# Performance work log

Hardware: AMD Instinct MI355X
Metric: run time of the kernel (lower is better)

Reference implementation:

```python
import jax, jax.numpy as jnp
import numpy as np

B, N, D, H, K, R = 128, 2048, 256, 16, 32, 16
LEAKY_SLOPE = 0.01


def setup_inputs() -> dict:
    key = jax.random.key(0)
    ks = jax.random.split(key, 8)
    s = 0.05
    inp = jax.random.normal(ks[0], (B * N, D), dtype=jnp.float32)
    batch_ids = jnp.repeat(jnp.arange(B, dtype=jnp.int32), N)  # equal-size graphs
    Wk = jax.random.normal(ks[1], (K, D), dtype=jnp.float32) * s
    Wq0 = jax.random.normal(ks[2], (H * K, D), dtype=jnp.float32) * s
    Wq1 = jax.random.normal(ks[3], (H * K, D), dtype=jnp.float32) * s
    We = jax.random.normal(ks[4], (R, D), dtype=jnp.float32) * s
    Wout = jax.random.normal(ks[5], (D, H * R), dtype=jnp.float32) * s
    bout = jax.random.normal(ks[6], (D,), dtype=jnp.float32) * s
    return {"inp": inp, "batch_ids": batch_ids, "Wk": Wk, "Wq0": Wq0,
            "Wq1": Wq1, "We": We, "Wout": Wout, "bout": bout}


def reference(inp, batch_ids, Wk, Wq0, Wq1, We, Wout, bout):
    b = int(jnp.max(batch_ids)) + 1  # number of graphs (static at trace time)
    d = inp.shape[-1]
    # global max pool per graph (torch_geometric global_max_pool)
    pooled = jax.ops.segment_max(inp, batch_ids, num_segments=b)  # [B, D]
    x = inp.reshape(b, -1, d)                                     # [B, N, D]
    keys = jnp.einsum('bnd,kd->bnk', x, Wk)                       # [B, N, K]

    def head_embed(Wq):
        q = (pooled @ Wq.T).reshape(b, H, K)                      # [B, H, K]
        logits = jnp.einsum('bhk,bnk->bhn', q, keys)              # [B, H, N]
        att = jax.nn.softmax(logits, axis=-1)
        feat = jnp.einsum('bhn,bnd->bhd', att, x)                 # [B, H, D]
        return jnp.einsum('bhd,rd->bhr', feat, We)                # [B, H, R]

    dx = (head_embed(Wq0) - head_embed(Wq1)).reshape(b, -1)       # [B, H*R]
    out = dx @ Wout.T + bout
    return jnp.where(out >= 0, out, LEAKY_SLOPE * out)            # LeakyReLU
```

## Files before the change

### kernel.cpp

```cpp
#include <hip/hip_runtime.h>
#include <math.h>

#define B_ 128
#define N_ 2048
#define D_ 256
#define NHEADS 32

#define POOLED_OFF 0
#define PHI_OFF    32768
#define PLO_OFF    557056
#define ML_OFF     1081344
#define FEATP_OFF  1114112
#define XHI_OFF    5308416
#define XLO_OFF    38862848

#define XHI_S 0
#define XLO_S 32768
#define ATT_S 0
#define XT_S  33280
#define STAT_S 53760

typedef __attribute__((ext_vector_type(8))) short short8;
typedef __attribute__((ext_vector_type(4))) float f32x4;

__device__ __forceinline__ void atomic_max_f32(float* addr, float v) {
    if (v >= 0.0f) atomicMax((int*)addr, __float_as_int(v + 0.0f));
    else           atomicMin((unsigned int*)addr, __float_as_uint(v));
}
__device__ __forceinline__ unsigned short f2bf(float f) {
    unsigned u = __float_as_uint(f);
    u += 0x7fff + ((u >> 16) & 1);
    return (unsigned short)(u >> 16);
}
__device__ __forceinline__ float bf2f(unsigned short h) {
    return __uint_as_float(((unsigned)h) << 16);
}
__device__ __forceinline__ unsigned pack2bf(float a, float b) {
    return (unsigned)f2bf(a) | ((unsigned)f2bf(b) << 16);
}

__global__ __launch_bounds__(256) void k_init(float* __restrict__ pooled) {
    pooled[blockIdx.x * 256 + threadIdx.x] = -INFINITY;
}

__global__ __launch_bounds__(256) void k_pool(const float* __restrict__ inp,
                                              float* __restrict__ pooled,
                                              unsigned short* __restrict__ xhi,
                                              unsigned short* __restrict__ xlo) {
    int b = blockIdx.x >> 4;
    int ch = blockIdx.x & 15;
    int t = threadIdx.x;
    int sub = t >> 6;
    int dq = (t & 63) * 4;
    const float* p = inp + ((size_t)(b * N_ + ch * 128 + sub)) * D_ + dq;
    size_t nodebase = (size_t)b * N_ + ch * 128 + sub;
    float4 m = {-INFINITY, -INFINITY, -INFINITY, -INFINITY};
#pragma unroll 4
    for (int i = 0; i < 32; ++i) {
        float4 v = *(const float4*)(p + (size_t)i * 4 * D_);
        m.x = fmaxf(m.x, v.x); m.y = fmaxf(m.y, v.y);
        m.z = fmaxf(m.z, v.z); m.w = fmaxf(m.w, v.w);
        size_t node = nodebase + (size_t)i * 4;
        ushort4 h4, l4;
        h4.x = f2bf(v.x); l4.x = f2bf(v.x - bf2f(h4.x));
        h4.y = f2bf(v.y); l4.y = f2bf(v.y - bf2f(h4.y));
        h4.z = f2bf(v.z); l4.z = f2bf(v.z - bf2f(h4.z));
        h4.w = f2bf(v.w); l4.w = f2bf(v.w - bf2f(h4.w));
        *(ushort4*)(xhi + node * D_ + dq) = h4;
        *(ushort4*)(xlo + node * D_ + dq) = l4;
    }
    __shared__ float sm[4 * 256];
    sm[sub * 256 + dq + 0] = m.x;
    sm[sub * 256 + dq + 1] = m.y;
    sm[sub * 256 + dq + 2] = m.z;
    sm[sub * 256 + dq + 3] = m.w;
    __syncthreads();
    float v = fmaxf(fmaxf(sm[t], sm[256 + t]), fmaxf(sm[512 + t], sm[768 + t]));
    atomic_max_f32(pooled + b * D_ + t, v);
}

__global__ __launch_bounds__(256) void k_qp(const float* __restrict__ pooled,
                                            const float* __restrict__ Wq0,
                                            const float* __restrict__ Wq1,
                                            const float* __restrict__ Wk,
                                            unsigned short* __restrict__ Phi,
                                            unsigned short* __restrict__ Plo) {
    __shared__ float pl[D_];
    __shared__ float ql[1024];
    int b = blockIdx.x, t = threadIdx.x;
    pl[t] = pooled[b * D_ + t];
    __syncthreads();
    for (int rep = 0; rep < 4; ++rep) {
        int idx = rep * 256 + t;
        const float* Wq = (idx < 512) ? Wq0 : Wq1;
        int row = idx & 511;
        const float4* wr = (const float4*)(Wq + (size_t)row * D_);
        float acc = 0.0f;
        for (int dqi = 0; dqi < 64; ++dqi) {
            float4 w = wr[dqi];
            const float* pp = &pl[dqi * 4];
            acc += w.x * pp[0] + w.y * pp[1] + w.z * pp[2] + w.w * pp[3];
        }
        ql[idx] = acc;
    }
    __syncthreads();
    float wk[32];
#pragma unroll
    for (int k = 0; k < 32; ++k) wk[k] = Wk[k * D_ + t];
    for (int j = 0; j < NHEADS; ++j) {
        const float* q = &ql[(j >> 4) * 512 + (j & 15) * 32];
        float acc = 0.0f;
#pragma unroll
        for (int k = 0; k < 32; ++k) acc = fmaf(q[k], wk[k], acc);
        unsigned short hi = f2bf(acc);
        unsigned short lo = f2bf(acc - bf2f(hi));
        Phi[((size_t)b * NHEADS + j) * D_ + t] = hi;
        Plo[((size_t)b * NHEADS + j) * D_ + t] = lo;
    }
}

__global__ __launch_bounds__(256) void k_attn(const unsigned short* __restrict__ xhi,
                                              const unsigned short* __restrict__ xlo,
                                              const unsigned short* __restrict__ Phi,
                                              const unsigned short* __restrict__ Plo,
                                              float* __restrict__ ml,
                                              float* __restrict__ featp) {
    __shared__ uint4 smem4[4096];
    unsigned char* smem = (unsigned char*)smem4;
    float* smax = (float*)(smem + STAT_S);
    float* ssum = (float*)(smem + STAT_S + 512);

    int b = blockIdx.x >> 2, ns = blockIdx.x & 3;
    int t = threadIdx.x;
    int w = t >> 6;
    int lane = t & 63;
    int lq = lane >> 4;
    int lm = lane & 15;
    size_t gnode0 = (size_t)b * N_ + ns * 512;

    f32x4 acc_s[8][2];
#pragma unroll
    for (int mt = 0; mt < 8; ++mt)
#pragma unroll
        for (int ht = 0; ht < 2; ++ht) acc_s[mt][ht] = (f32x4){0.f, 0.f, 0.f, 0.f};

    int srow = t >> 2, sseg = t & 3;
    for (int dc = 0; dc < 8; ++dc) {
        int d0 = dc * 32;
        short8 bh[2], bl[2];
#pragma unroll
        for (int ht = 0; ht < 2; ++ht) {
            size_t poff = ((size_t)b * NHEADS + ht * 16 + lm) * D_ + d0 + lq * 8;
            bh[ht] = *(const short8*)(Phi + poff);
            bl[ht] = *(const short8*)(Plo + poff);
        }
        const unsigned short* gxh = xhi + (gnode0 + srow) * D_ + d0 + sseg * 8;
        const unsigned short* gxl = xlo + (gnode0 + srow) * D_ + d0 + sseg * 8;
        __syncthreads();
#pragma unroll
        for (int i = 0; i < 8; ++i) {
            *(uint4*)(smem + XHI_S + (size_t)(srow + i * 64) * 64 + sseg * 16) =
                *(const uint4*)(gxh + (size_t)i * 64 * D_);
            *(uint4*)(smem + XLO_S + (size_t)(srow + i * 64) * 64 + sseg * 16) =
                *(const uint4*)(gxl + (size_t)i * 64 * D_);
        }
        __syncthreads();
#pragma unroll
        for (int mt = 0; mt < 8; ++mt) {
            size_t roff = (size_t)(w * 128 + mt * 16 + lm) * 64 + lq * 16;
            short8 ah = *(const short8*)(smem + XHI_S + roff);
            short8 al = *(const short8*)(smem + XLO_S + roff);
#pragma unroll
            for (int ht = 0; ht < 2; ++ht) {
                acc_s[mt][ht] = __builtin_amdgcn_mfma_f32_16x16x32_bf16(ah, bh[ht], acc_s[mt][ht], 0, 0, 0);
                acc_s[mt][ht] = __builtin_amdgcn_mfma_f32_16x16x32_bf16(ah, bl[ht], acc_s[mt][ht], 0, 0, 0);
                acc_s[mt][ht] = __builtin_amdgcn_mfma_f32_16x16x32_bf16(al, bh[ht], acc_s[mt][ht], 0, 0, 0);
            }
        }
    }
    __syncthreads();

    float bm[2];
#pragma unroll
    for (int ht = 0; ht < 2; ++ht) {
        float m = -INFINITY;
#pragma unroll
        for (int mt = 0; mt < 8; ++mt) {
            m = fmaxf(m, fmaxf(fmaxf(acc_s[mt][ht][0], acc_s[mt][ht][1]),
                               fmaxf(acc_s[mt][ht][2], acc_s[mt][ht][3])));
        }
        m = fmaxf(m, __shfl_xor(m, 16));
        m = fmaxf(m, __shfl_xor(m, 32));
        if (lane < 16) smax[w * 32 + ht * 16 + lane] = m;
    }
    __syncthreads();
#pragma unroll
    for (int ht = 0; ht < 2; ++ht) {
        bm[ht] = fmaxf(fmaxf(smax[0 * 32 + ht * 16 + lm], smax[1 * 32 + ht * 16 + lm]),
                       fmaxf(smax[2 * 32 + ht * 16 + lm], smax[3 * 32 + ht * 16 + lm]));
    }
#pragma unroll
    for (int ht = 0; ht < 2; ++ht) {
        float s = 0.0f;
#pragma unroll
        for (int mt = 0; mt < 8; ++mt) {
            float e0 = __expf(acc_s[mt][ht][0] - bm[ht]);
            float e1 = __expf(acc_s[mt][ht][1] - bm[ht]);
            float e2 = __expf(acc_s[mt][ht][2] - bm[ht]);
            float e3 = __expf(acc_s[mt][ht][3] - bm[ht]);
            s += (e0 + e1) + (e2 + e3);
            uint2 pk;
            pk.x = pack2bf(e0, e1);
            pk.y = pack2bf(e2, e3);
            *(uint2*)(smem + ATT_S + (size_t)(ht * 16 + lm) * 1040 +
                      (size_t)(w * 128 + mt * 16 + lq * 4) * 2) = pk;
        }
        s += __shfl_xor(s, 16);
        s += __shfl_xor(s, 32);
        if (lane < 16) ssum[w * 32 + ht * 16 + lane] = s;
    }
    __syncthreads();
    if (t < 32) {
        float mB = fmaxf(fmaxf(smax[t], smax[32 + t]), fmaxf(smax[64 + t], smax[96 + t]));
        float l = ssum[t] + ssum[32 + t] + ssum[64 + t] + ssum[96 + t];
        float* mlp = ml + (((size_t)b * NHEADS + t) * 4 + ns) * 2;
        mlp[0] = mB;
        mlp[1] = l;
    }
    __syncthreads();

    f32x4 acc_o[2][4];
#pragma unroll
    for (int mt = 0; mt < 2; ++mt)
#pragma unroll
        for (int dt = 0; dt < 4; ++dt) acc_o[mt][dt] = (f32x4){0.f, 0.f, 0.f, 0.f};

    int db = t & 31, nb = t >> 5;
    for (int c = 0; c < 16; ++c) {
        const unsigned short* gx = xhi + (gnode0 + c * 32 + nb * 4) * D_ + db * 8;
        uint4 R0 = *(const uint4*)(gx);
        uint4 R1 = *(const uint4*)(gx + D_);
        uint4 R2 = *(const uint4*)(gx + 2 * D_);
        uint4 R3 = *(const uint4*)(gx + 3 * D_);
        const unsigned* r0 = (const unsigned*)&R0;
        const unsigned* r1 = (const unsigned*)&R1;
        const unsigned* r2 = (const unsigned*)&R2;
        const unsigned* r3 = (const unsigned*)&R3;
        uint2 T[8];
#pragma unroll
        for (int c2 = 0; c2 < 4; ++c2) {
            T[2 * c2 + 0].x = __builtin_amdgcn_perm(r1[c2], r0[c2], 0x05040100u);
            T[2 * c2 + 0].y = __builtin_amdgcn_perm(r3[c2], r2[c2], 0x05040100u);
            T[2 * c2 + 1].x = __builtin_amdgcn_perm(r1[c2], r0[c2], 0x07060302u);
            T[2 * c2 + 1].y = __builtin_amdgcn_perm(r3[c2], r2[c2], 0x07060302u);
        }
        __syncthreads();
#pragma unroll
        for (int j = 0; j < 8; ++j) {
            int jj = (j + db) & 7;
            *(uint2*)(smem + XT_S + (size_t)(db * 8 + jj) * 80 + nb * 8) = T[jj];
        }
        __syncthreads();
        short8 a0 = *(const short8*)(smem + ATT_S + (size_t)lm * 1040 + (size_t)(c * 32 + lq * 8) * 2);
        short8 a1 = *(const short8*)(smem + ATT_S + (size_t)(16 + lm) * 1040 + (size_t)(c * 32 + lq * 8) * 2);
#pragma unroll
        for (int dt = 0; dt < 4; ++dt) {
            short8 bf = *(const short8*)(smem + XT_S + (size_t)(w * 64 + dt * 16 + lm) * 80 + lq * 16);
            acc_o[0][dt] = __builtin_amdgcn_mfma_f32_16x16x32_bf16(a0, bf, acc_o[0][dt], 0, 0, 0);
            acc_o[1][dt] = __builtin_amdgcn_mfma_f32_16x16x32_bf16(a1, bf, acc_o[1][dt], 0, 0, 0);
        }
    }
    float* fb = featp + ((size_t)(ns * B_ + b)) * D_ * NHEADS;
#pragma unroll
    for (int mt = 0; mt < 2; ++mt)
#pragma unroll
        for (int dt = 0; dt < 4; ++dt) {
            int d = w * 64 + dt * 16 + lm;
            int h0 = mt * 16 + lq * 4;
            *(f32x4*)(fb + (size_t)d * NHEADS + h0) = acc_o[mt][dt];
        }
}

__global__ __launch_bounds__(256) void k_out(const float* __restrict__ featp,
                                             const float* __restrict__ ml,
                                             const float* __restrict__ We,
                                             const float* __restrict__ Wout,
                                             const float* __restrict__ bout,
                                             float* __restrict__ out) {
    __shared__ float f[NHEADS * 257];
    __shared__ float bhrs[512];
    __shared__ float dxs[256];
    __shared__ float wns[4 * 32];
    __shared__ float linv2[32];
    int b = blockIdx.x, t = threadIdx.x;
    if (t < 32) {
        const float* mlb = ml + ((size_t)b * NHEADS + t) * 8;
        float M = fmaxf(fmaxf(mlb[0], mlb[2]), fmaxf(mlb[4], mlb[6]));
        float e0 = __expf(mlb[0] - M), e1 = __expf(mlb[2] - M);
        float e2 = __expf(mlb[4] - M), e3 = __expf(mlb[6] - M);
        float L = e0 * mlb[1] + e1 * mlb[3] + e2 * mlb[5] + e3 * mlb[7];
        wns[0 * 32 + t] = e0; wns[1 * 32 + t] = e1;
        wns[2 * 32 + t] = e2; wns[3 * 32 + t] = e3;
        linv2[t] = 1.0f / L;
    }
    __syncthreads();
    float fj[32];
#pragma unroll
    for (int j = 0; j < 32; ++j) fj[j] = 0.0f;
#pragma unroll
    for (int ns = 0; ns < 4; ++ns) {
        const float* fp = featp + ((size_t)(ns * B_ + b) * D_ + t) * NHEADS;
#pragma unroll
        for (int j4 = 0; j4 < 8; ++j4) {
            float4 v = *(const float4*)(fp + j4 * 4);
            fj[j4 * 4 + 0] += wns[ns * 32 + j4 * 4 + 0] * v.x;
            fj[j4 * 4 + 1] += wns[ns * 32 + j4 * 4 + 1] * v.y;
            fj[j4 * 4 + 2] += wns[ns * 32 + j4 * 4 + 2] * v.z;
            fj[j4 * 4 + 3] += wns[ns * 32 + j4 * 4 + 3] * v.w;
        }
    }
#pragma unroll
    for (int j = 0; j < 32; ++j) f[j * 257 + t] = fj[j] * linv2[j];
    __syncthreads();
    for (int rep = 0; rep < 2; ++rep) {
        int idx = rep * 256 + t;
        int j = idx >> 4, r = idx & 15;
        const float* wrow = We + (size_t)r * D_;
        const float* ff = &f[j * 257];
        float acc = 0.0f;
        for (int d = 0; d < D_; ++d) acc = fmaf(ff[d], wrow[d], acc);
        bhrs[idx] = acc;
    }
    __syncthreads();
    {
        int h = t >> 4, r = t & 15;
        dxs[t] = bhrs[h * 16 + r] - bhrs[(16 + h) * 16 + r];
    }
    __syncthreads();
    float acc = bout[t];
    const float* wrow = Wout + (size_t)t * 256;
    for (int c = 0; c < 256; ++c) acc = fmaf(dxs[c], wrow[c], acc);
    out[(size_t)b * D_ + t] = acc >= 0.0f ? acc : 0.01f * acc;
}

extern "C" void kernel_launch(void* const* d_in, const int* in_sizes, int n_in,
                              void* d_out, int out_size, void* d_ws, size_t ws_size,
                              hipStream_t stream) {
    const float* inp  = (const float*)d_in[0];
    const float* Wk   = (const float*)d_in[2];
    const float* Wq0  = (const float*)d_in[3];
    const float* Wq1  = (const float*)d_in[4];
    const float* We   = (const float*)d_in[5];
    const float* Wout = (const float*)d_in[6];
    const float* bout = (const float*)d_in[7];
    float* out = (float*)d_out;
    float* ws  = (float*)d_ws;
    float* pooled = ws + POOLED_OFF;
    unsigned short* Phi = (unsigned short*)(ws + PHI_OFF);
    unsigned short* Plo = (unsigned short*)(ws + PLO_OFF);
    float* ml     = ws + ML_OFF;
    float* featp  = ws + FEATP_OFF;
    unsigned short* xhi = (unsigned short*)(ws + XHI_OFF);
    unsigned short* xlo = (unsigned short*)(ws + XLO_OFF);

    k_init<<<dim3(128), dim3(256), 0, stream>>>(pooled);
    k_pool<<<dim3(2048), dim3(256), 0, stream>>>(inp, pooled, xhi, xlo);
    k_qp<<<dim3(128), dim3(256), 0, stream>>>(pooled, Wq0, Wq1, Wk, Phi, Plo);
    k_attn<<<dim3(512), dim3(256), 0, stream>>>(xhi, xlo, Phi, Plo, ml, featp);
    k_out<<<dim3(128), dim3(256), 0, stream>>>(featp, ml, We, Wout, bout, out);
}
```

Baseline: 607.2 us.

## Fuse bf16 split into attention kernel and drop global xhi/xlo buffers

The attention kernel now reads the fp32 input directly and splits it into bf16 hi/lo parts inside a swizzled LDS tile. This removes the large global write and re-read of the xhi/xlo intermediates. Work is split into 16 chunks of 128 nodes per graph with 512-thread blocks and about 141 KB of dynamic LDS, which likely allows only one block per CU. Pooling writes per-chunk partial maxima that k_qp reduces, replacing the atomics and the init kernel. The cost is a 4x larger featp partial buffer and scalar strided LDS reads for the transposed operand.

```diff
diff --git a/kernel.cpp b/kernel.cpp
--- a/kernel.cpp
+++ b/kernel.cpp
@@ -5,28 +5,25 @@
 #define N_ 2048
 #define D_ 256
 #define NHEADS 32
-
-#define POOLED_OFF 0
-#define PHI_OFF    32768
-#define PLO_OFF    557056
-#define ML_OFF     1081344
-#define FEATP_OFF  1114112
-#define XHI_OFF    5308416
-#define XLO_OFF    38862848
-
-#define XHI_S 0
-#define XLO_S 32768
-#define ATT_S 0
-#define XT_S  33280
-#define STAT_S 53760
+#define CHUNK 128
+#define NCH 16
+
+#define POOLEDP_OFF 0
+#define PHI_OFF     524288
+#define PLO_OFF     1048576
+#define ML_OFF      1572864
+#define FEATP_OFF   1703936
+
+#define XHI_S  0
+#define XLO_S  65536
+#define ATT_S  131072
+#define SMAX_S 139776
+#define SSUM_S 140800
+#define LDS_BYTES 141824
 
 typedef __attribute__((ext_vector_type(8))) short short8;
 typedef __attribute__((ext_vector_type(4))) float f32x4;
 
-__device__ __forceinline__ void atomic_max_f32(float* addr, float v) {
-    if (v >= 0.0f) atomicMax((int*)addr, __float_as_int(v + 0.0f));
-    else           atomicMin((unsigned int*)addr, __float_as_uint(v));
-}
 __device__ __forceinline__ unsigned short f2bf(float f) {
     unsigned u = __float_as_uint(f);
     u += 0x7fff + ((u >> 16) & 1);
@@ -38,36 +35,24 @@
 __device__ __forceinline__ unsigned pack2bf(float a, float b) {
     return (unsigned)f2bf(a) | ((unsigned)f2bf(b) << 16);
 }
-
-__global__ __launch_bounds__(256) void k_init(float* __restrict__ pooled) {
-    pooled[blockIdx.x * 256 + threadIdx.x] = -INFINITY;
+__device__ __forceinline__ unsigned xsw(int row) {
+    return (unsigned)((row ^ (row >> 3)) & 7) << 4;
 }
 
 __global__ __launch_bounds__(256) void k_pool(const float* __restrict__ inp,
-                                              float* __restrict__ pooled,
-                                              unsigned short* __restrict__ xhi,
-                                              unsigned short* __restrict__ xlo) {
+                                              float* __restrict__ pooledp) {
     int b = blockIdx.x >> 4;
     int ch = blockIdx.x & 15;
     int t = threadIdx.x;
     int sub = t >> 6;
     int dq = (t & 63) * 4;
     const float* p = inp + ((size_t)(b * N_ + ch * 128 + sub)) * D_ + dq;
-    size_t nodebase = (size_t)b * N_ + ch * 128 + sub;
     float4 m = {-INFINITY, -INFINITY, -INFINITY, -INFINITY};
 #pragma unroll 4
     for (int i = 0; i < 32; ++i) {
         float4 v = *(const float4*)(p + (size_t)i * 4 * D_);
         m.x = fmaxf(m.x, v.x); m.y = fmaxf(m.y, v.y);
         m.z = fmaxf(m.z, v.z); m.w = fmaxf(m.w, v.w);
-        size_t node = nodebase + (size_t)i * 4;
-        ushort4 h4, l4;
-        h4.x = f2bf(v.x); l4.x = f2bf(v.x - bf2f(h4.x));
-        h4.y = f2bf(v.y); l4.y = f2bf(v.y - bf2f(h4.y));
-        h4.z = f2bf(v.z); l4.z = f2bf(v.z - bf2f(h4.z));
-        h4.w = f2bf(v.w); l4.w = f2bf(v.w - bf2f(h4.w));
-        *(ushort4*)(xhi + node * D_ + dq) = h4;
-        *(ushort4*)(xlo + node * D_ + dq) = l4;
     }
     __shared__ float sm[4 * 256];
     sm[sub * 256 + dq + 0] = m.x;
@@ -76,10 +61,10 @@
     sm[sub * 256 + dq + 3] = m.w;
     __syncthreads();
     float v = fmaxf(fmaxf(sm[t], sm[256 + t]), fmaxf(sm[512 + t], sm[768 + t]));
-    atomic_max_f32(pooled + b * D_ + t, v);
-}
-
-__global__ __launch_bounds__(256) void k_qp(const float* __restrict__ pooled,
+    pooledp[((size_t)ch * B_ + b) * 256 + t] = v;
+}
+
+__global__ __launch_bounds__(256) void k_qp(const float* __restrict__ pooledp,
                                             const float* __restrict__ Wq0,
                                             const float* __restrict__ Wq1,
                                             const float* __restrict__ Wk,
@@ -88,7 +73,11 @@
     __shared__ float pl[D_];
     __shared__ float ql[1024];
     int b = blockIdx.x, t = threadIdx.x;
-    pl[t] = pooled[b * D_ + t];
+    float pv = -INFINITY;
+#pragma unroll
+    for (int i = 0; i < 16; ++i)
+        pv = fmaxf(pv, pooledp[((size_t)i * B_ + b) * 256 + t]);
+    pl[t] = pv;
     __syncthreads();
     for (int rep = 0; rep < 4; ++rep) {
         int idx = rep * 256 + t;
@@ -119,76 +108,69 @@
     }
 }
 
-__global__ __launch_bounds__(256) void k_attn(const unsigned short* __restrict__ xhi,
-                                              const unsigned short* __restrict__ xlo,
-                                              const unsigned short* __restrict__ Phi,
-                                              const unsigned short* __restrict__ Plo,
-                                              float* __restrict__ ml,
-                                              float* __restrict__ featp) {
-    __shared__ uint4 smem4[4096];
-    unsigned char* smem = (unsigned char*)smem4;
-    float* smax = (float*)(smem + STAT_S);
-    float* ssum = (float*)(smem + STAT_S + 512);
-
-    int b = blockIdx.x >> 2, ns = blockIdx.x & 3;
+__global__ __launch_bounds__(512, 2) void k_attn(const float* __restrict__ inp,
+                                                 const unsigned short* __restrict__ Phi,
+                                                 const unsigned short* __restrict__ Plo,
+                                                 float* __restrict__ ml,
+                                                 float* __restrict__ featp) {
+    extern __shared__ unsigned char smem[];
+    float* smax = (float*)(smem + SMAX_S);
+    float* ssum = (float*)(smem + SSUM_S);
+
+    int b = blockIdx.x >> 4, ns = blockIdx.x & 15;
     int t = threadIdx.x;
     int w = t >> 6;
     int lane = t & 63;
     int lq = lane >> 4;
     int lm = lane & 15;
-    size_t gnode0 = (size_t)b * N_ + ns * 512;
-
-    f32x4 acc_s[8][2];
-#pragma unroll
-    for (int mt = 0; mt < 8; ++mt)
-#pragma unroll
-        for (int ht = 0; ht < 2; ++ht) acc_s[mt][ht] = (f32x4){0.f, 0.f, 0.f, 0.f};
-
-    int srow = t >> 2, sseg = t & 3;
+    size_t gnode0 = (size_t)b * N_ + (size_t)ns * CHUNK;
+
+#pragma unroll
+    for (int i = 0; i < 16; ++i) {
+        int row = i * 8 + w;
+        float4 v = *(const float4*)(inp + (gnode0 + row) * D_ + lane * 4);
+        ushort4 h4, l4;
+        h4.x = f2bf(v.x); l4.x = f2bf(v.x - bf2f(h4.x));
+        h4.y = f2bf(v.y); l4.y = f2bf(v.y - bf2f(h4.y));
+        h4.z = f2bf(v.z); l4.z = f2bf(v.z - bf2f(h4.z));
+        h4.w = f2bf(v.w); l4.w = f2bf(v.w - bf2f(h4.w));
+        unsigned byteoff = (unsigned)row * 512u + (((unsigned)lane * 8u) ^ xsw(row));
+        *(ushort4*)(smem + XHI_S + byteoff) = h4;
+        *(ushort4*)(smem + XLO_S + byteoff) = l4;
+    }
+    __syncthreads();
+
+    f32x4 acc_s[2];
+    acc_s[0] = (f32x4){0.f, 0.f, 0.f, 0.f};
+    acc_s[1] = (f32x4){0.f, 0.f, 0.f, 0.f};
+    int arow = w * 16 + lm;
+    unsigned abase = (unsigned)arow * 512u;
+    unsigned asl = xsw(arow);
+#pragma unroll
     for (int dc = 0; dc < 8; ++dc) {
-        int d0 = dc * 32;
         short8 bh[2], bl[2];
 #pragma unroll
         for (int ht = 0; ht < 2; ++ht) {
-            size_t poff = ((size_t)b * NHEADS + ht * 16 + lm) * D_ + d0 + lq * 8;
+            size_t poff = ((size_t)b * NHEADS + ht * 16 + lm) * D_ + dc * 32 + lq * 8;
             bh[ht] = *(const short8*)(Phi + poff);
             bl[ht] = *(const short8*)(Plo + poff);
         }
-        const unsigned short* gxh = xhi + (gnode0 + srow) * D_ + d0 + sseg * 8;
-        const unsigned short* gxl = xlo + (gnode0 + srow) * D_ + d0 + sseg * 8;
-        __syncthreads();
-#pragma unroll
-        for (int i = 0; i < 8; ++i) {
-            *(uint4*)(smem + XHI_S + (size_t)(srow + i * 64) * 64 + sseg * 16) =
-                *(const uint4*)(gxh + (size_t)i * 64 * D_);
-            *(uint4*)(smem + XLO_S + (size_t)(srow + i * 64) * 64 + sseg * 16) =
-                *(const uint4*)(gxl + (size_t)i * 64 * D_);
-        }
-        __syncthreads();
-#pragma unroll
-        for (int mt = 0; mt < 8; ++mt) {
-            size_t roff = (size_t)(w * 128 + mt * 16 + lm) * 64 + lq * 16;
-            short8 ah = *(const short8*)(smem + XHI_S + roff);
-            short8 al = *(const short8*)(smem + XLO_S + roff);
-#pragma unroll
-            for (int ht = 0; ht < 2; ++ht) {
-                acc_s[mt][ht] = __builtin_amdgcn_mfma_f32_16x16x32_bf16(ah, bh[ht], acc_s[mt][ht], 0, 0, 0);
-                acc_s[mt][ht] = __builtin_amdgcn_mfma_f32_16x16x32_bf16(ah, bl[ht], acc_s[mt][ht], 0, 0, 0);
-                acc_s[mt][ht] = __builtin_amdgcn_mfma_f32_16x16x32_bf16(al, bh[ht], acc_s[mt][ht], 0, 0, 0);
-            }
-        }
-    }
-    __syncthreads();
+        unsigned doff = (((unsigned)(dc * 32 + lq * 8)) * 2u) ^ asl;
+        short8 ah = *(const short8*)(smem + XHI_S + abase + doff);
+        short8 al = *(const short8*)(smem + XLO_S + abase + doff);
+#pragma unroll
+        for (int ht = 0; ht < 2; ++ht) {
+            acc_s[ht] = __builtin_amdgcn_mfma_f32_16x16x32_bf16(ah, bh[ht], acc_s[ht], 0, 0, 0);
+            acc_s[ht] = __builtin_amdgcn_mfma_f32_16x16x32_bf16(ah, bl[ht], acc_s[ht], 0, 0, 0);
+            acc_s[ht] = __builtin_amdgcn_mfma_f32_16x16x32_bf16(al, bh[ht], acc_s[ht], 0, 0, 0);
+        }
+    }
 
     float bm[2];
 #pragma unroll
     for (int ht = 0; ht < 2; ++ht) {
-        float m = -INFINITY;
-#pragma unroll
-        for (int mt = 0; mt < 8; ++mt) {
-            m = fmaxf(m, fmaxf(fmaxf(acc_s[mt][ht][0], acc_s[mt][ht][1]),
-                               fmaxf(acc_s[mt][ht][2], acc_s[mt][ht][3])));
-        }
+        float m = fmaxf(fmaxf(acc_s[ht][0], acc_s[ht][1]),
+                        fmaxf(acc_s[ht][2], acc_s[ht][3]));
         m = fmaxf(m, __shfl_xor(m, 16));
         m = fmaxf(m, __shfl_xor(m, 32));
         if (lane < 16) smax[w * 32 + ht * 16 + lane] = m;
@@ -196,88 +178,74 @@
     __syncthreads();
 #pragma unroll
     for (int ht = 0; ht < 2; ++ht) {
-        bm[ht] = fmaxf(fmaxf(smax[0 * 32 + ht * 16 + lm], smax[1 * 32 + ht * 16 + lm]),
-                       fmaxf(smax[2 * 32 + ht * 16 + lm], smax[3 * 32 + ht * 16 + lm]));
+        float mm = smax[ht * 16 + lm];
+#pragma unroll
+        for (int w2 = 1; w2 < 8; ++w2) mm = fmaxf(mm, smax[w2 * 32 + ht * 16 + lm]);
+        bm[ht] = mm;
     }
 #pragma unroll
     for (int ht = 0; ht < 2; ++ht) {
-        float s = 0.0f;
-#pragma unroll
-        for (int mt = 0; mt < 8; ++mt) {
-            float e0 = __expf(acc_s[mt][ht][0] - bm[ht]);
-            float e1 = __expf(acc_s[mt][ht][1] - bm[ht]);
-            float e2 = __expf(acc_s[mt][ht][2] - bm[ht]);
-            float e3 = __expf(acc_s[mt][ht][3] - bm[ht]);
-            s += (e0 + e1) + (e2 + e3);
-            uint2 pk;
-            pk.x = pack2bf(e0, e1);
-            pk.y = pack2bf(e2, e3);
-            *(uint2*)(smem + ATT_S + (size_t)(ht * 16 + lm) * 1040 +
-                      (size_t)(w * 128 + mt * 16 + lq * 4) * 2) = pk;
-        }
+        float e0 = __expf(acc_s[ht][0] - bm[ht]);
+        float e1 = __expf(acc_s[ht][1] - bm[ht]);
+        float e2 = __expf(acc_s[ht][2] - bm[ht]);
+        float e3 = __expf(acc_s[ht][3] - bm[ht]);
+        float s = (e0 + e1) + (e2 + e3);
+        uint2 pk;
+        pk.x = pack2bf(e0, e1);
+        pk.y = pack2bf(e2, e3);
+        *(uint2*)(smem + ATT_S + (size_t)(ht * 16 + lm) * 272 + w * 32 + lq * 8) = pk;
         s += __shfl_xor(s, 16);
         s += __shfl_xor(s, 32);
         if (lane < 16) ssum[w * 32 + ht * 16 + lane] = s;
     }
     __syncthreads();
     if (t < 32) {
-        float mB = fmaxf(fmaxf(smax[t], smax[32 + t]), fmaxf(smax[64 + t], smax[96 + t]));
-        float l = ssum[t] + ssum[32 + t] + ssum[64 + t] + ssum[96 + t];
-        float* mlp = ml + (((size_t)b * NHEADS + t) * 4 + ns) * 2;
+        float mB = smax[t];
+        float l = ssum[t];
+#pragma unroll
+        for (int w2 = 1; w2 < 8; ++w2) {
+            mB = fmaxf(mB, smax[w2 * 32 + t]);
+            l += ssum[w2 * 32 + t];
+        }
+        float* mlp = ml + ((size_t)(b * NHEADS + t) * NCH + ns) * 2;
         mlp[0] = mB;
         mlp[1] = l;
     }
-    __syncthreads();
-
-    f32x4 acc_o[2][4];
-#pragma unroll
-    for (int mt = 0; mt < 2; ++mt)
-#pragma unroll
-        for (int dt = 0; dt < 4; ++dt) acc_o[mt][dt] = (f32x4){0.f, 0.f, 0.f, 0.f};
-
-    int db = t & 31, nb = t >> 5;
-    for (int c = 0; c < 16; ++c) {
-        const unsigned short* gx = xhi + (gnode0 + c * 32 + nb * 4) * D_ + db * 8;
-        uint4 R0 = *(const uint4*)(gx);
-        uint4 R1 = *(const uint4*)(gx + D_);
-        uint4 R2 = *(const uint4*)(gx + 2 * D_);
-        uint4 R3 = *(const uint4*)(gx + 3 * D_);
-        const unsigned* r0 = (const unsigned*)&R0;
-        const unsigned* r1 = (const unsigned*)&R1;
-        const unsigned* r2 = (const unsigned*)&R2;
-        const unsigned* r3 = (const unsigned*)&R3;
-        uint2 T[8];
-#pragma unroll
-        for (int c2 = 0; c2 < 4; ++c2) {
-            T[2 * c2 + 0].x = __builtin_amdgcn_perm(r1[c2], r0[c2], 0x05040100u);
-            T[2 * c2 + 0].y = __builtin_amdgcn_perm(r3[c2], r2[c2], 0x05040100u);
-            T[2 * c2 + 1].x = __builtin_amdgcn_perm(r1[c2], r0[c2], 0x07060302u);
-            T[2 * c2 + 1].y = __builtin_amdgcn_perm(r3[c2], r2[c2], 0x07060302u);
-        }
-        __syncthreads();
-#pragma unroll
-        for (int j = 0; j < 8; ++j) {
-            int jj = (j + db) & 7;
-            *(uint2*)(smem + XT_S + (size_t)(db * 8 + jj) * 80 + nb * 8) = T[jj];
-        }
-        __syncthreads();
-        short8 a0 = *(const short8*)(smem + ATT_S + (size_t)lm * 1040 + (size_t)(c * 32 + lq * 8) * 2);
-        short8 a1 = *(const short8*)(smem + ATT_S + (size_t)(16 + lm) * 1040 + (size_t)(c * 32 + lq * 8) * 2);
-#pragma unroll
-        for (int dt = 0; dt < 4; ++dt) {
-            short8 bf = *(const short8*)(smem + XT_S + (size_t)(w * 64 + dt * 16 + lm) * 80 + lq * 16);
+
+    f32x4 acc_o[2][2];
+#pragma unroll
+    for (int ht = 0; ht < 2; ++ht)
+#pragma unroll
+        for (int dt = 0; dt < 2; ++dt) acc_o[ht][dt] = (f32x4){0.f, 0.f, 0.f, 0.f};
+
+    int d0w = w * 32;
+#pragma unroll
+    for (int c = 0; c < 4; ++c) {
+        short8 a0 = *(const short8*)(smem + ATT_S + (size_t)lm * 272 + c * 64 + lq * 16);
+        short8 a1 = *(const short8*)(smem + ATT_S + (size_t)(16 + lm) * 272 + c * 64 + lq * 16);
+#pragma unroll
+        for (int dt = 0; dt < 2; ++dt) {
+            unsigned d2 = (unsigned)(d0w + dt * 16 + lm) * 2u;
+            int n0 = c * 32 + lq * 8;
+            short8 bf;
+#pragma unroll
+            for (int j = 0; j < 8; ++j) {
+                int n = n0 + j;
+                unsigned byteoff = (unsigned)n * 512u + (d2 ^ xsw(n));
+                bf[j] = *(const short*)(smem + XHI_S + byteoff);
+            }
             acc_o[0][dt] = __builtin_amdgcn_mfma_f32_16x16x32_bf16(a0, bf, acc_o[0][dt], 0, 0, 0);
             acc_o[1][dt] = __builtin_amdgcn_mfma_f32_16x16x32_bf16(a1, bf, acc_o[1][dt], 0, 0, 0);
         }
     }
     float* fb = featp + ((size_t)(ns * B_ + b)) * D_ * NHEADS;
 #pragma unroll
-    for (int mt = 0; mt < 2; ++mt)
-#pragma unroll
-        for (int dt = 0; dt < 4; ++dt) {
-            int d = w * 64 + dt * 16 + lm;
-            int h0 = mt * 16 + lq * 4;
-            *(f32x4*)(fb + (size_t)d * NHEADS + h0) = acc_o[mt][dt];
+    for (int ht = 0; ht < 2; ++ht)
+#pragma unroll
+        for (int dt = 0; dt < 2; ++dt) {
+            int d = d0w + dt * 16 + lm;
+            int h0 = ht * 16 + lq * 4;
+            *(f32x4*)(fb + (size_t)d * NHEADS + h0) = acc_o[ht][dt];
         }
 }
 
@@ -290,25 +258,28 @@
     __shared__ float f[NHEADS * 257];
     __shared__ float bhrs[512];
     __shared__ float dxs[256];
-    __shared__ float wns[4 * 32];
+    __shared__ float wns[NCH * 32];
     __shared__ float linv2[32];
     int b = blockIdx.x, t = threadIdx.x;
     if (t < 32) {
-        const float* mlb = ml + ((size_t)b * NHEADS + t) * 8;
-        float M = fmaxf(fmaxf(mlb[0], mlb[2]), fmaxf(mlb[4], mlb[6]));
-        float e0 = __expf(mlb[0] - M), e1 = __expf(mlb[2] - M);
-        float e2 = __expf(mlb[4] - M), e3 = __expf(mlb[6] - M);
-        float L = e0 * mlb[1] + e1 * mlb[3] + e2 * mlb[5] + e3 * mlb[7];
-        wns[0 * 32 + t] = e0; wns[1 * 32 + t] = e1;
-        wns[2 * 32 + t] = e2; wns[3 * 32 + t] = e3;
+        const float* mlb = ml + ((size_t)b * NHEADS + t) * (NCH * 2);
+        float M = mlb[0];
+#pragma unroll
+        for (int i = 1; i < NCH; ++i) M = fmaxf(M, mlb[2 * i]);
+        float L = 0.0f;
+#pragma unroll
+        for (int i = 0; i < NCH; ++i) {
+            float e = __expf(mlb[2 * i] - M);
+            wns[i * 32 + t] = e;
+            L += e * mlb[2 * i + 1];
+        }
         linv2[t] = 1.0f / L;
     }
     __syncthreads();
     float fj[32];
 #pragma unroll
     for (int j = 0; j < 32; ++j) fj[j] = 0.0f;
-#pragma unroll
-    for (int ns = 0; ns < 4; ++ns) {
+    for (int ns = 0; ns < NCH; ++ns) {
         const float* fp = featp + ((size_t)(ns * B_ + b) * D_ + t) * NHEADS;
 #pragma unroll
         for (int j4 = 0; j4 < 8; ++j4) {
@@ -355,17 +326,22 @@
     const float* bout = (const float*)d_in[7];
     float* out = (float*)d_out;
     float* ws  = (float*)d_ws;
-    float* pooled = ws + POOLED_OFF;
+    float* pooledp = ws + POOLEDP_OFF;
     unsigned short* Phi = (unsigned short*)(ws + PHI_OFF);
     unsigned short* Plo = (unsigned short*)(ws + PLO_OFF);
     float* ml     = ws + ML_OFF;
     float* featp  = ws + FEATP_OFF;
-    unsigned short* xhi = (unsigned short*)(ws + XHI_OFF);
-    unsigned short* xlo = (unsigned short*)(ws + XLO_OFF);
-
-    k_init<<<dim3(128), dim3(256), 0, stream>>>(pooled);
-    k_pool<<<dim3(2048), dim3(256), 0, stream>>>(inp, pooled, xhi, xlo);
-    k_qp<<<dim3(128), dim3(256), 0, stream>>>(pooled, Wq0, Wq1, Wk, Phi, Plo);
-    k_attn<<<dim3(512), dim3(256), 0, stream>>>(xhi, xlo, Phi, Plo, ml, featp);
+
+    static int lds_set = 0;
+    if (!lds_set) {
+        (void)hipFuncSetAttribute((const void*)k_attn,
+                                  hipFuncAttributeMaxDynamicSharedMemorySize,
+                                  LDS_BYTES);
+        lds_set = 1;
+    }
+
+    k_pool<<<dim3(2048), dim3(256), 0, stream>>>(inp, pooledp);
+    k_qp<<<dim3(128), dim3(256), 0, stream>>>(pooledp, Wq0, Wq1, Wk, Phi, Plo);
+    k_attn<<<dim3(2048), dim3(512), LDS_BYTES, stream>>>(inp, Phi, Plo, ml, featp);
     k_out<<<dim3(128), dim3(256), 0, stream>>>(featp, ml, We, Wout, bout, out);
 }
```

After: 613.5 us. Within noise of the previous version (+1.0%).
